# Kernel optimization log

Hardware: AMD Instinct MI355X
Metric: run time of the kernel (lower is better)

Reference implementation:

```python
import jax, jax.numpy as jnp
import numpy as np


def setup_inputs() -> dict:
    key = jax.random.key(0)
    k1, k2 = jax.random.split(key)
    q, k, d5 = 128, 2048, 768
    return {
        "tgt": jax.random.normal(k1, (q, d5), dtype=jnp.float32),
        "memory": jax.random.normal(k2, (k, d5), dtype=jnp.float32),
        "seq_len": 32,
    }


def reference(tgt, memory, seq_len):
    q, d5 = tgt.shape
    k, _ = memory.shape
    z = d5 // seq_len  # per-token sub-dim
    query_t = tgt.reshape(q, seq_len, z)    # [q, t, d]
    key_m = memory.reshape(k, seq_len, z)   # [k, s, d]
    # Full late-interaction similarity tensor [q, k, s, t]
    score = jnp.einsum('qtd,ksd->qkst', query_t, key_m)
    # max over memory tokens (s) and over query tokens (t), concat, mean
    pooled = jnp.concatenate((score.max(axis=2), score.max(axis=3)), axis=-1)  # [q, k, 2*seq_len]
    score_p = jax.nn.sigmoid(pooled.mean(axis=-1))  # [q, k]
    return (score_p, score_p)
```

## Files before the change

kernel.cpp:

```cpp
#include <hip/hip_runtime.h>
#include <hip/hip_bf16.h>

typedef __bf16 bf16x8 __attribute__((ext_vector_type(8)));
typedef short  s16x4  __attribute__((ext_vector_type(4)));
typedef float  f32x16 __attribute__((ext_vector_type(16)));
typedef int    i32x2  __attribute__((ext_vector_type(2)));

constexpr int QN  = 128;
constexpr int KN  = 2048;
constexpr int D5  = 768;
constexpr int SL  = 32;
constexpr int ZD  = 24;
constexpr int KCH = 16;
constexpr int WPB = 8;

#if __has_builtin(__builtin_amdgcn_mfma_f32_32x32x8bf16_1k)
#define HAVE_MFMA_X8 1
#else
#define HAVE_MFMA_X8 0
#endif

#if __has_builtin(__builtin_amdgcn_permlane32_swap)
#define HAVE_PERMLANE32 1
#else
#define HAVE_PERMLANE32 0
#endif

static __device__ __forceinline__ float max3f(float a, float b, float c) {
    return fmaxf(fmaxf(a, b), c);
}

static __device__ __forceinline__ float redmax16(const f32x16& a) {
    float x0 = max3f(a[0],  a[1],  a[2]);
    float x1 = max3f(a[3],  a[4],  a[5]);
    float x2 = max3f(a[6],  a[7],  a[8]);
    float x3 = max3f(a[9],  a[10], a[11]);
    float x4 = max3f(a[12], a[13], a[14]);
    float y0 = max3f(x0, x1, x2);
    float y1 = max3f(x3, x4, a[15]);
    return fmaxf(y0, y1);
}

static __device__ __forceinline__ float halfmax(float m) {
#if HAVE_PERMLANE32
    i32x2 pr = __builtin_amdgcn_permlane32_swap(__builtin_bit_cast(int, m),
                                                __builtin_bit_cast(int, m),
                                                false, false);
    return fmaxf(__builtin_bit_cast(float, pr[0]), __builtin_bit_cast(float, pr[1]));
#else
    return fmaxf(m, __shfl_xor(m, 32));
#endif
}

#if HAVE_MFMA_X8
static __device__ __forceinline__ short f2bfbits(float x) {
    __bf16 b = (__bf16)x;
    return __builtin_bit_cast(short, b);
}
#endif

__global__ __launch_bounds__(512, 4) void matcher_kernel(const float* __restrict__ tgt,
                                                         const float* __restrict__ mem,
                                                         float* __restrict__ out)
{
    __shared__ __align__(16) __bf16 Kf[KCH * 768];
    __shared__ float vbuf[WPB][KCH * 32];

    const int tid = threadIdx.x;
    const int qg  = blockIdx.x;
    const int kc  = blockIdx.y;
    const int k0  = kc * KCH;

    {
        const int r  = tid;
        const int kl = r >> 5;
        const int s  = r & 31;
        const float* src = mem + (size_t)(k0 + kl) * D5 + s * ZD;
        float tv[24];
#pragma unroll
        for (int j = 0; j < 6; ++j) ((float4*)tv)[j] = ((const float4*)src)[j];
        bf16x8 a, b, c;
#pragma unroll
        for (int j = 0; j < 8; ++j) {
            a[j] = (__bf16)tv[j];
            b[j] = (__bf16)tv[8 + j];
            c[j] = (__bf16)tv[16 + j];
        }
        __bf16* base = Kf + kl * 768;
        *(bf16x8*)(base +        s * 8)  = a;
        *(bf16x8*)(base + (32 +  s) * 8) = b;
        *(bf16x8*)(base + 512 +  s * 8)  = c;
    }

    const int lane = tid & 63;
    const int wv   = tid >> 6;
    const int t    = lane & 31;
    const int h    = lane >> 5;
    const int q    = qg * WPB + wv;

    const float4* p4 = (const float4*)(tgt + (size_t)q * D5 + t * ZD);
    bf16x8 aQ0;
    {
        float4 u0 = p4[2 * h], u1 = p4[2 * h + 1];
        aQ0[0] = (__bf16)u0.x; aQ0[1] = (__bf16)u0.y; aQ0[2] = (__bf16)u0.z; aQ0[3] = (__bf16)u0.w;
        aQ0[4] = (__bf16)u1.x; aQ0[5] = (__bf16)u1.y; aQ0[6] = (__bf16)u1.z; aQ0[7] = (__bf16)u1.w;
    }
#if HAVE_MFMA_X8
    s16x4 aQ1;
    {
        float4 w = p4[4 + h];
        aQ1[0] = f2bfbits(w.x); aQ1[1] = f2bfbits(w.y);
        aQ1[2] = f2bfbits(w.z); aQ1[3] = f2bfbits(w.w);
    }
#else
    bf16x8 aQ1;
    if (h == 0) {
        float4 w0 = p4[4], w1 = p4[5];
        aQ1[0] = (__bf16)w0.x; aQ1[1] = (__bf16)w0.y; aQ1[2] = (__bf16)w0.z; aQ1[3] = (__bf16)w0.w;
        aQ1[4] = (__bf16)w1.x; aQ1[5] = (__bf16)w1.y; aQ1[6] = (__bf16)w1.z; aQ1[7] = (__bf16)w1.w;
    } else {
#pragma unroll
        for (int j = 0; j < 8; ++j) aQ1[j] = (__bf16)0.0f;
    }
#endif

    f32x16 zacc;
#pragma unroll
    for (int i = 0; i < 16; ++i) zacc[i] = 0.0f;

    __syncthreads();

    float* vb = vbuf[wv];

#pragma unroll
    for (int kl = 0; kl < KCH; ++kl) {
        const __bf16* lb = Kf + kl * 768;
        bf16x8 bK0 = *(const bf16x8*)(lb + lane * 8);
#if HAVE_MFMA_X8
        s16x4 bK1 = *(const s16x4*)(lb + 512 + t * 8 + h * 4);

        f32x16 accS = __builtin_amdgcn_mfma_f32_32x32x16_bf16(aQ0, bK0, zacc, 0, 0, 0);
        accS = __builtin_amdgcn_mfma_f32_32x32x8bf16_1k(aQ1, bK1, accS, 0, 0, 0);
        f32x16 accT = __builtin_amdgcn_mfma_f32_32x32x16_bf16(bK0, aQ0, zacc, 0, 0, 0);
        accT = __builtin_amdgcn_mfma_f32_32x32x8bf16_1k(bK1, aQ1, accT, 0, 0, 0);
#else
        bf16x8 bK1 = *(const bf16x8*)(lb + 512 + t * 8);

        f32x16 accS = __builtin_amdgcn_mfma_f32_32x32x16_bf16(aQ0, bK0, zacc, 0, 0, 0);
        accS        = __builtin_amdgcn_mfma_f32_32x32x16_bf16(aQ1, bK1, accS, 0, 0, 0);
        f32x16 accT = __builtin_amdgcn_mfma_f32_32x32x16_bf16(bK0, aQ0, zacc, 0, 0, 0);
        accT        = __builtin_amdgcn_mfma_f32_32x32x16_bf16(bK1, aQ1, accT, 0, 0, 0);
#endif
        float m1 = halfmax(redmax16(accS));
        float m2 = halfmax(redmax16(accT));
        float v = m1 + m2;
        if (h == 0) vb[(kl << 5) + (t ^ kl)] = v;
    }

    {
        const int p    = lane & 15;
        const int half = (lane >> 4) & 1;
        float x[16];
#pragma unroll
        for (int i = 0; i < 16; ++i)
            x[i] = vb[(p << 5) + ((half << 4) + i ^ p)];
        float s0 = (x[0] + x[1]) + (x[2] + x[3]);
        float s1 = (x[4] + x[5]) + (x[6] + x[7]);
        float s2 = (x[8] + x[9]) + (x[10] + x[11]);
        float s3 = (x[12] + x[13]) + (x[14] + x[15]);
        float sum = (s0 + s1) + (s2 + s3);
        sum += __shfl_xor(sum, 16);
        float r = 1.0f / (1.0f + __expf(-sum * (1.0f / 64.0f)));
        if (lane < 16) {
            const int idx = q * KN + k0 + p;
            out[idx] = r;
            out[idx + QN * KN] = r;
        }
    }
}

extern "C" void kernel_launch(void* const* d_in, const int* in_sizes, int n_in,
                              void* d_out, int out_size, void* d_ws, size_t ws_size,
                              hipStream_t stream)
{
    const float* tgt = (const float*)d_in[0];
    const float* mem = (const float*)d_in[1];
    float* out = (float*)d_out;
    dim3 grid(QN / WPB, KN / KCH);
    matcher_kernel<<<grid, 512, 0, stream>>>(tgt, mem, out);
}
```

Measured before the change: 92.19 us.

## Tile each wave over 4 queries x 4 keys with register-held operands

Each wave now handles a 4-query by 4-key sub-tile instead of one query over all 16 keys. It loads its 4 key fragments from LDS once into registers and reuses them across 4 queries, so the per-pair LDS reads of the previous loop go away. The cost is more VGPRs for the query and key fragment arrays, which may reduce occupancy under the 512-thread launch bound. Query loads from global memory become four per wave instead of one.

```diff
diff --git a/kernel.cpp b/kernel.cpp
--- a/kernel.cpp
+++ b/kernel.cpp
@@ -64,7 +64,7 @@
                                                          float* __restrict__ out)
 {
     __shared__ __align__(16) __bf16 Kf[KCH * 768];
-    __shared__ float vbuf[WPB][KCH * 32];
+    __shared__ float vbuf[WPB][16 * 32];
 
     const int tid = threadIdx.x;
     const int qg  = blockIdx.x;
@@ -96,33 +96,42 @@
     const int wv   = tid >> 6;
     const int t    = lane & 31;
     const int h    = lane >> 5;
-    const int q    = qg * WPB + wv;
-
-    const float4* p4 = (const float4*)(tgt + (size_t)q * D5 + t * ZD);
-    bf16x8 aQ0;
-    {
+    const int g    = wv >> 2;
+    const int ks   = wv & 3;
+    const int qb   = qg * WPB + g * 4;
+    const int kb   = ks * 4;
+
+    bf16x8 aQ0[4];
+#if HAVE_MFMA_X8
+    s16x4 aQ1[4];
+#else
+    bf16x8 aQ1[4];
+#endif
+#pragma unroll
+    for (int qi = 0; qi < 4; ++qi) {
+        const float4* p4 = (const float4*)(tgt + (size_t)(qb + qi) * D5 + t * ZD);
         float4 u0 = p4[2 * h], u1 = p4[2 * h + 1];
-        aQ0[0] = (__bf16)u0.x; aQ0[1] = (__bf16)u0.y; aQ0[2] = (__bf16)u0.z; aQ0[3] = (__bf16)u0.w;
-        aQ0[4] = (__bf16)u1.x; aQ0[5] = (__bf16)u1.y; aQ0[6] = (__bf16)u1.z; aQ0[7] = (__bf16)u1.w;
-    }
-#if HAVE_MFMA_X8
-    s16x4 aQ1;
-    {
+        aQ0[qi][0] = (__bf16)u0.x; aQ0[qi][1] = (__bf16)u0.y;
+        aQ0[qi][2] = (__bf16)u0.z; aQ0[qi][3] = (__bf16)u0.w;
+        aQ0[qi][4] = (__bf16)u1.x; aQ0[qi][5] = (__bf16)u1.y;
+        aQ0[qi][6] = (__bf16)u1.z; aQ0[qi][7] = (__bf16)u1.w;
+#if HAVE_MFMA_X8
         float4 w = p4[4 + h];
-        aQ1[0] = f2bfbits(w.x); aQ1[1] = f2bfbits(w.y);
-        aQ1[2] = f2bfbits(w.z); aQ1[3] = f2bfbits(w.w);
-    }
-#else
-    bf16x8 aQ1;
-    if (h == 0) {
-        float4 w0 = p4[4], w1 = p4[5];
-        aQ1[0] = (__bf16)w0.x; aQ1[1] = (__bf16)w0.y; aQ1[2] = (__bf16)w0.z; aQ1[3] = (__bf16)w0.w;
-        aQ1[4] = (__bf16)w1.x; aQ1[5] = (__bf16)w1.y; aQ1[6] = (__bf16)w1.z; aQ1[7] = (__bf16)w1.w;
-    } else {
-#pragma unroll
-        for (int j = 0; j < 8; ++j) aQ1[j] = (__bf16)0.0f;
-    }
-#endif
+        aQ1[qi][0] = f2bfbits(w.x); aQ1[qi][1] = f2bfbits(w.y);
+        aQ1[qi][2] = f2bfbits(w.z); aQ1[qi][3] = f2bfbits(w.w);
+#else
+        if (h == 0) {
+            float4 w0 = p4[4], w1 = p4[5];
+            aQ1[qi][0] = (__bf16)w0.x; aQ1[qi][1] = (__bf16)w0.y;
+            aQ1[qi][2] = (__bf16)w0.z; aQ1[qi][3] = (__bf16)w0.w;
+            aQ1[qi][4] = (__bf16)w1.x; aQ1[qi][5] = (__bf16)w1.y;
+            aQ1[qi][6] = (__bf16)w1.z; aQ1[qi][7] = (__bf16)w1.w;
+        } else {
+#pragma unroll
+            for (int j = 0; j < 8; ++j) aQ1[qi][j] = (__bf16)0.0f;
+        }
+#endif
+    }
 
     f32x16 zacc;
 #pragma unroll
@@ -130,31 +139,44 @@
 
     __syncthreads();
 
+    bf16x8 bK0[4];
+#if HAVE_MFMA_X8
+    s16x4 bK1[4];
+#else
+    bf16x8 bK1[4];
+#endif
+#pragma unroll
+    for (int ki = 0; ki < 4; ++ki) {
+        const __bf16* lb = Kf + (kb + ki) * 768;
+        bK0[ki] = *(const bf16x8*)(lb + lane * 8);
+#if HAVE_MFMA_X8
+        bK1[ki] = *(const s16x4*)(lb + 512 + t * 8 + h * 4);
+#else
+        bK1[ki] = *(const bf16x8*)(lb + 512 + t * 8);
+#endif
+    }
+
     float* vb = vbuf[wv];
 
-#pragma unroll
-    for (int kl = 0; kl < KCH; ++kl) {
-        const __bf16* lb = Kf + kl * 768;
-        bf16x8 bK0 = *(const bf16x8*)(lb + lane * 8);
-#if HAVE_MFMA_X8
-        s16x4 bK1 = *(const s16x4*)(lb + 512 + t * 8 + h * 4);
-
-        f32x16 accS = __builtin_amdgcn_mfma_f32_32x32x16_bf16(aQ0, bK0, zacc, 0, 0, 0);
-        accS = __builtin_amdgcn_mfma_f32_32x32x8bf16_1k(aQ1, bK1, accS, 0, 0, 0);
-        f32x16 accT = __builtin_amdgcn_mfma_f32_32x32x16_bf16(bK0, aQ0, zacc, 0, 0, 0);
-        accT = __builtin_amdgcn_mfma_f32_32x32x8bf16_1k(bK1, aQ1, accT, 0, 0, 0);
-#else
-        bf16x8 bK1 = *(const bf16x8*)(lb + 512 + t * 8);
-
-        f32x16 accS = __builtin_amdgcn_mfma_f32_32x32x16_bf16(aQ0, bK0, zacc, 0, 0, 0);
-        accS        = __builtin_amdgcn_mfma_f32_32x32x16_bf16(aQ1, bK1, accS, 0, 0, 0);
-        f32x16 accT = __builtin_amdgcn_mfma_f32_32x32x16_bf16(bK0, aQ0, zacc, 0, 0, 0);
-        accT        = __builtin_amdgcn_mfma_f32_32x32x16_bf16(bK1, aQ1, accT, 0, 0, 0);
+#pragma unroll 4
+    for (int pr = 0; pr < 16; ++pr) {
+        const int qi = pr >> 2;
+        const int ki = pr & 3;
+#if HAVE_MFMA_X8
+        f32x16 accS = __builtin_amdgcn_mfma_f32_32x32x16_bf16(aQ0[qi], bK0[ki], zacc, 0, 0, 0);
+        accS = __builtin_amdgcn_mfma_f32_32x32x8bf16_1k(aQ1[qi], bK1[ki], accS, 0, 0, 0);
+        f32x16 accT = __builtin_amdgcn_mfma_f32_32x32x16_bf16(bK0[ki], aQ0[qi], zacc, 0, 0, 0);
+        accT = __builtin_amdgcn_mfma_f32_32x32x8bf16_1k(bK1[ki], aQ1[qi], accT, 0, 0, 0);
+#else
+        f32x16 accS = __builtin_amdgcn_mfma_f32_32x32x16_bf16(aQ0[qi], bK0[ki], zacc, 0, 0, 0);
+        accS        = __builtin_amdgcn_mfma_f32_32x32x16_bf16(aQ1[qi], bK1[ki], accS, 0, 0, 0);
+        f32x16 accT = __builtin_amdgcn_mfma_f32_32x32x16_bf16(bK0[ki], aQ0[qi], zacc, 0, 0, 0);
+        accT        = __builtin_amdgcn_mfma_f32_32x32x16_bf16(bK1[ki], aQ1[qi], accT, 0, 0, 0);
 #endif
         float m1 = halfmax(redmax16(accS));
         float m2 = halfmax(redmax16(accT));
         float v = m1 + m2;
-        if (h == 0) vb[(kl << 5) + (t ^ kl)] = v;
+        if (h == 0) vb[(pr << 5) + (t ^ pr)] = v;
     }
 
     {
@@ -163,7 +185,7 @@
         float x[16];
 #pragma unroll
         for (int i = 0; i < 16; ++i)
-            x[i] = vb[(p << 5) + ((half << 4) + i ^ p)];
+            x[i] = vb[(p << 5) + ((((half << 4) + i)) ^ p)];
         float s0 = (x[0] + x[1]) + (x[2] + x[3]);
         float s1 = (x[4] + x[5]) + (x[6] + x[7]);
         float s2 = (x[8] + x[9]) + (x[10] + x[11]);
@@ -172,7 +194,9 @@
         sum += __shfl_xor(sum, 16);
         float r = 1.0f / (1.0f + __expf(-sum * (1.0f / 64.0f)));
         if (lane < 16) {
-            const int idx = q * KN + k0 + p;
+            const int q = qb + (p >> 2);
+            const int k = k0 + kb + (p & 3);
+            const int idx = q * KN + k;
             out[idx] = r;
             out[idx + QN * KN] = r;
         }
```

Result: slower. 144.8 us (+57.0%).
